# Optimization experiments

Measured on AMD Instinct MI355X. Metric: run time of the kernel, lower is better.

## Reference

```python
import jax, jax.numpy as jnp
import numpy as np

N = 100000
E = 1600000
IN_FEATS = 128
H_FEATS = 128
NUM_CLASSES = 64
BN_EPS = 1e-5


def setup_inputs() -> dict:
    key = jax.random.key(0)
    ks = jax.random.split(key, 16)
    inp = {
        "in_feat": jax.random.normal(ks[0], (N, IN_FEATS), dtype=jnp.float32),
        "src": jax.random.randint(ks[1], (E,), 0, N, dtype=jnp.int64),
        "dst": jax.random.randint(ks[2], (E,), 0, N, dtype=jnp.int64),
        # GraphConv weights (glorot-ish scale) and biases
        "W0": jax.random.normal(ks[3], (IN_FEATS, H_FEATS), dtype=jnp.float32) / np.sqrt(IN_FEATS),
        "b0": jnp.zeros((H_FEATS,), dtype=jnp.float32),
        "W1": jax.random.normal(ks[4], (H_FEATS, H_FEATS), dtype=jnp.float32) / np.sqrt(H_FEATS),
        "b1": jnp.zeros((H_FEATS,), dtype=jnp.float32),
        "W2": jax.random.normal(ks[5], (H_FEATS, NUM_CLASSES), dtype=jnp.float32) / np.sqrt(H_FEATS),
        "b2": jnp.zeros((NUM_CLASSES,), dtype=jnp.float32),
        # BatchNorm affine params
        "gamma0": jnp.ones((H_FEATS,), dtype=jnp.float32),
        "beta0": jnp.zeros((H_FEATS,), dtype=jnp.float32),
        "gamma1": jnp.ones((H_FEATS,), dtype=jnp.float32),
        "beta1": jnp.zeros((H_FEATS,), dtype=jnp.float32),
    }
    return inp


def _graph_conv(src, dst, h, W, b):
    # DGL GraphConv, norm='both': D_dst^{-1/2} A (D_src^{-1/2} h W) + b
    ones = jnp.ones((src.shape[0],), dtype=h.dtype)
    deg_out = jnp.clip(jax.ops.segment_sum(ones, src, num_segments=N), 1.0)
    deg_in = jnp.clip(jax.ops.segment_sum(ones, dst, num_segments=N), 1.0)
    h = h * jax.lax.rsqrt(deg_out)[:, None]
    h = h @ W  # mult weight before aggregation (same math either way)
    agg = jax.ops.segment_sum(h[src], dst, num_segments=N)  # SpMM
    return agg * jax.lax.rsqrt(deg_in)[:, None] + b


def _batch_norm(h, gamma, beta):
    # BatchNorm1d in training mode: biased batch stats over the node axis
    mean = jnp.mean(h, axis=0)
    var = jnp.mean(jnp.square(h - mean), axis=0)
    return (h - mean) * jax.lax.rsqrt(var + BN_EPS) * gamma + beta


def reference(in_feat, src, dst, W0, b0, W1, b1, W2, b2, gamma0, beta0, gamma1, beta1):
    h = _graph_conv(src, dst, in_feat, W0, b0)
    h = jax.nn.relu(_batch_norm(h, gamma0, beta0))  # dropout p=0 -> identity
    h = _graph_conv(src, dst, h, W1, b1)
    h = jax.nn.relu(_batch_norm(h, gamma1, beta1))
    return _graph_conv(src, dst, h, W2, b2)
```

## Files before the change

### kernel.cpp

```cpp
#include <hip/hip_runtime.h>

#define NFEAT 128
#define BT 2048
#define BSH 9
#define BSZ 512
#define NP 256

typedef __attribute__((ext_vector_type(8))) short short8v;
typedef __attribute__((ext_vector_type(4))) float float4v;

static inline size_t align_up(size_t x, size_t a) { return (x + a - 1) & ~(a - 1); }

__device__ inline unsigned short f2bf(float f) {
  unsigned u = __float_as_uint(f);
  u += 0x7FFF + ((u >> 16) & 1);
  return (unsigned short)(u >> 16);
}
__device__ inline unsigned pack2bf(float lo, float hi) {
  return ((unsigned)f2bf(lo)) | (((unsigned)f2bf(hi)) << 16);
}
__device__ inline float bflo(unsigned u) { return __uint_as_float(u << 16); }
__device__ inline float bfhi(unsigned u) { return __uint_as_float(u & 0xFFFF0000u); }
__device__ inline int goff(const int* __restrict__ off, const int* __restrict__ bscan, int i) {
  return off[i] + bscan[i >> 9];
}

__global__ __launch_bounds__(256) void k_bcount(const int* __restrict__ src,
                                                const int* __restrict__ dst,
                                                int* __restrict__ cnt, int E, int nb, int NBK) {
  __shared__ int hD[256], hS[256];
  const int t = threadIdx.x, b = blockIdx.x;
  hD[t] = 0; hS[t] = 0;
  __syncthreads();
  const int e0 = b * BT, e1 = min(E, e0 + BT);
  for (int e = e0 + t; e < e1; e += 256) {
    atomicAdd(&hD[dst[e] >> BSH], 1);
    atomicAdd(&hS[src[e] >> BSH], 1);
  }
  __syncthreads();
  if (t < NBK) {
    cnt[t * nb + b] = hD[t];
    cnt[(NBK + t) * nb + b] = hS[t];
  }
}

__global__ __launch_bounds__(512) void k_scanA(const int* __restrict__ in,
                                               int* __restrict__ out,
                                               int* __restrict__ bsum, int n) {
  __shared__ int tmp[512];
  const int t = threadIdx.x;
  const int i = blockIdx.x * 512 + t;
  int v = (i < n) ? in[i] : 0;
  tmp[t] = v;
  __syncthreads();
  for (int off = 1; off < 512; off <<= 1) {
    int y = (t >= off) ? tmp[t - off] : 0;
    __syncthreads();
    tmp[t] += y;
    __syncthreads();
  }
  int incl = tmp[t];
  if (i < n) out[i] = incl - v;
  if (t == 511) bsum[blockIdx.x] = incl;
}

__global__ __launch_bounds__(1024) void k_scanB(const int* __restrict__ bsum,
                                                int* __restrict__ bscan, int nb1) {
  __shared__ int tmp[1024];
  const int t = threadIdx.x;
  int v = (t < nb1) ? bsum[t] : 0;
  tmp[t] = v;
  __syncthreads();
  for (int off = 1; off < 1024; off <<= 1) {
    int y = (t >= off) ? tmp[t - off] : 0;
    __syncthreads();
    tmp[t] += y;
    __syncthreads();
  }
  bscan[t] = tmp[t] - v;
}

__global__ __launch_bounds__(256) void k_bplace(const int* __restrict__ src,
                                                const int* __restrict__ dst,
                                                const int* __restrict__ off,
                                                const int* __restrict__ bscan,
                                                int* __restrict__ buf, int E, int nb, int NBK) {
  __shared__ int cD[256], cS[256];
  const int t = threadIdx.x, b = blockIdx.x;
  if (t < NBK) {
    cD[t] = goff(off, bscan, t * nb + b);
    cS[t] = goff(off, bscan, (NBK + t) * nb + b);
  }
  __syncthreads();
  const int e0 = b * BT, e1 = min(E, e0 + BT);
  for (int e = e0 + t; e < e1; e += 256) {
    int s = src[e];
    int d = dst[e];
    int pD = atomicAdd(&cD[d >> BSH], 1);
    buf[pD] = ((d & (BSZ - 1)) << 17) | s;
    int pS = atomicAdd(&cS[s >> BSH], 1);
    buf[pS] = s;
  }
}

__global__ __launch_bounds__(256) void k_bcsr_deg(const int* __restrict__ buf,
                                                  const int* __restrict__ off,
                                                  const int* __restrict__ bscan,
                                                  int* __restrict__ row_ptr,
                                                  float* __restrict__ rsq_in,
                                                  float* __restrict__ rsq_out,
                                                  int* __restrict__ col,
                                                  int E, int nb, int NBK, int N) {
  const int k = blockIdx.x, t = threadIdx.x;
  __shared__ int cnt[BSZ];
  __shared__ int sc[BSZ];
  __shared__ int part[64];
  const int lo = goff(off, bscan, k * nb);
  const int hi = (k + 1 < NBK) ? goff(off, bscan, (k + 1) * nb) : E;
  cnt[t] = 0; cnt[t + 256] = 0;
  __syncthreads();
  for (int e = lo + t; e < hi; e += 256) atomicAdd(&cnt[((unsigned)buf[e]) >> 17], 1);
  __syncthreads();
  if (t < 64) {
    int r = 0;
#pragma unroll
    for (int j = 0; j < 8; ++j) r += cnt[t * 8 + j];
    part[t] = r;
  }
  __syncthreads();
  if (t == 0) {
    int run = 0;
    for (int i = 0; i < 64; ++i) { int v = part[i]; part[i] = run; run += v; }
  }
  __syncthreads();
  if (t < 64) {
    int run = part[t];
#pragma unroll
    for (int j = 0; j < 8; ++j) { int v = cnt[t * 8 + j]; sc[t * 8 + j] = run; run += v; }
  }
  __syncthreads();
  for (int idx = t; idx < BSZ; idx += 256) {
    int n = (k << BSH) + idx;
    if (n < N) {
      row_ptr[n] = lo + sc[idx];
      int c = cnt[idx]; if (c < 1) c = 1;
      rsq_in[n] = 1.0f / sqrtf((float)c);
    }
    cnt[idx] = sc[idx];
  }
  if (k == NBK - 1 && t == 0) row_ptr[N] = E;
  __syncthreads();
  for (int e = lo + t; e < hi; e += 256) {
    int w = buf[e];
    int p = atomicAdd(&cnt[((unsigned)w) >> 17], 1);
    col[lo + p] = w & 0x1FFFF;
  }
  __syncthreads();
  cnt[t] = 0; cnt[t + 256] = 0;
  __syncthreads();
  const int lo2 = goff(off, bscan, (NBK + k) * nb);
  const int hi2 = (k + 1 < NBK) ? goff(off, bscan, (NBK + k + 1) * nb) : 2 * E;
  for (int e = lo2 + t; e < hi2; e += 256) atomicAdd(&cnt[buf[e] & (BSZ - 1)], 1);
  __syncthreads();
  for (int idx = t; idx < BSZ; idx += 256) {
    int n = (k << BSH) + idx;
    if (n < N) {
      int c = cnt[idx]; if (c < 1) c = 1;
      rsq_out[n] = 1.0f / sqrtf((float)c);
    }
  }
}

__global__ __launch_bounds__(256) void k_wprep(const float* __restrict__ W0,
                                               const float* __restrict__ W1,
                                               const float* __restrict__ W2,
                                               unsigned short* __restrict__ Wt0,
                                               unsigned short* __restrict__ Wt1,
                                               unsigned short* __restrict__ Wt2) {
  int t = blockIdx.x * 256 + threadIdx.x;
  if (t < 16384) {
    int c = t >> 7, k = t & 127;
    Wt0[c * 128 + k] = f2bf(W0[k * 128 + c]);
  } else if (t < 32768) {
    int u = t - 16384;
    int c = u >> 7, k = u & 127;
    Wt1[c * 128 + k] = f2bf(W1[k * 128 + c]);
  } else if (t < 40960) {
    int u = t - 32768;
    int c = u >> 7, k = u & 127;
    Wt2[c * 128 + k] = f2bf(W2[k * 64 + c]);
  }
}

template <int CC>
__global__ __launch_bounds__(256) void k_gemm_mfma(
    const float* __restrict__ X32, const unsigned short* __restrict__ Xbf,
    const unsigned short* __restrict__ Wt,
    unsigned short* __restrict__ Ybf, const float* __restrict__ rsq_out,
    const float* __restrict__ bnscale, const float* __restrict__ bnshift,
    int Nrows, int mode) {
  constexpr int XBYTES = 64 * 256;
  constexpr int WBYTES = CC * 256;
  __shared__ __align__(16) char lds[XBYTES + WBYTES];
  const int tid = threadIdx.x;
  const int rowBase = blockIdx.x * 64;

  for (int u = tid; u < CC * 16; u += 256) {
    int c = u >> 4, kq = u & 15;
    uint4 v = *(const uint4*)(Wt + c * 128 + kq * 8);
    int byte = (c * 256 + kq * 16) ^ ((c & 7) << 4);
    *(uint4*)(&lds[XBYTES + byte]) = v;
  }
  if (mode == 0) {
#pragma unroll
    for (int i = 0; i < 8; ++i) {
      int u = tid + i * 256;
      int r = u >> 5, kq = u & 31;
      int gr = rowBase + r;
      float4 v = make_float4(0.f, 0.f, 0.f, 0.f);
      if (gr < Nrows) v = *(const float4*)(X32 + (size_t)gr * 128 + kq * 4);
      ushort4 o;
      o.x = f2bf(v.x); o.y = f2bf(v.y); o.z = f2bf(v.z); o.w = f2bf(v.w);
      int byte = (r * 256 + kq * 8) ^ ((r & 7) << 4);
      *(ushort4*)(&lds[byte]) = o;
    }
  } else {
#pragma unroll
    for (int i = 0; i < 4; ++i) {
      int u = tid + i * 256;
      int r = u >> 4, kq = u & 15;
      int gr = rowBase + r;
      uint4 v = make_uint4(0, 0, 0, 0);
      if (gr < Nrows) v = *(const uint4*)(Xbf + (size_t)gr * 128 + kq * 8);
      float f0 = bflo(v.x), f1 = bfhi(v.x), f2 = bflo(v.y), f3 = bfhi(v.y);
      float f4 = bflo(v.z), f5 = bfhi(v.z), f6 = bflo(v.w), f7 = bfhi(v.w);
      const float4 sA = *(const float4*)(bnscale + kq * 8);
      const float4 sB = *(const float4*)(bnscale + kq * 8 + 4);
      const float4 hA = *(const float4*)(bnshift + kq * 8);
      const float4 hB = *(const float4*)(bnshift + kq * 8 + 4);
      f0 = fmaxf(f0 * sA.x + hA.x, 0.f); f1 = fmaxf(f1 * sA.y + hA.y, 0.f);
      f2 = fmaxf(f2 * sA.z + hA.z, 0.f); f3 = fmaxf(f3 * sA.w + hA.w, 0.f);
      f4 = fmaxf(f4 * sB.x + hB.x, 0.f); f5 = fmaxf(f5 * sB.y + hB.y, 0.f);
      f6 = fmaxf(f6 * sB.z + hB.z, 0.f); f7 = fmaxf(f7 * sB.w + hB.w, 0.f);
      uint4 o;
      o.x = pack2bf(f0, f1); o.y = pack2bf(f2, f3);
      o.z = pack2bf(f4, f5); o.w = pack2bf(f6, f7);
      int byte = (r * 256 + kq * 16) ^ ((r & 7) << 4);
      *(uint4*)(&lds[byte]) = o;
    }
  }
  __syncthreads();

  const int wv = tid >> 6;
  const int l = tid & 63;
  const int l16 = l & 15, lk = l >> 4;

  short8v a[4];
  const int arow = wv * 16 + l16;
#pragma unroll
  for (int kk = 0; kk < 4; ++kk) {
    int byte = (arow * 256 + kk * 64 + lk * 16) ^ ((arow & 7) << 4);
    a[kk] = *(const short8v*)(&lds[byte]);
  }

  float4v acc[CC / 16];
#pragma unroll
  for (int ct = 0; ct < CC / 16; ++ct) acc[ct] = (float4v){0.f, 0.f, 0.f, 0.f};

#pragma unroll
  for (int ct = 0; ct < CC / 16; ++ct) {
    const int col = ct * 16 + l16;
#pragma unroll
    for (int kk = 0; kk < 4; ++kk) {
      int byte = XBYTES + ((col * 256 + kk * 64 + lk * 16) ^ ((col & 7) << 4));
      short8v b = *(const short8v*)(&lds[byte]);
      acc[ct] = __builtin_amdgcn_mfma_f32_16x16x32_bf16(a[kk], b, acc[ct], 0, 0, 0);
    }
  }

  const int row0 = rowBase + wv * 16 + lk * 4;
  float scr[4];
#pragma unroll
  for (int r = 0; r < 4; ++r) scr[r] = (row0 + r < Nrows) ? rsq_out[row0 + r] : 0.f;
#pragma unroll
  for (int ct = 0; ct < CC / 16; ++ct) {
#pragma unroll
    for (int r = 0; r < 4; ++r) {
      int row = row0 + r;
      if (row < Nrows)
        Ybf[(size_t)row * CC + ct * 16 + l16] = f2bf(acc[ct][r] * scr[r]);
    }
  }
}

template <int F, int OUT_BF>
__global__ __launch_bounds__(256) void k_spmm2(const int* __restrict__ row_ptr,
                                               const int* __restrict__ colidx,
                                               const unsigned short* __restrict__ xW,
                                               void* __restrict__ outv,
                                               const float* __restrict__ rsq_in,
                                               const float* __restrict__ bias, int Nrows) {
  constexpr int FL = F / 8;
  constexpr int G = 64 / FL;
  const int node = blockIdx.x * 4 + (threadIdx.x >> 6);
  if (node >= Nrows) return;
  const int l = threadIdx.x & 63;
  const int fl = l % FL, g = l / FL;
  const int e0 = row_ptr[node];
  const int e1 = row_ptr[node + 1];
  float acc[8] = {};
  int e = e0 + g;
  for (; e + 3 * G < e1; e += 4 * G) {
    int s0 = colidx[e];
    int s1 = colidx[e + G];
    int s2 = colidx[e + 2 * G];
    int s3 = colidx[e + 3 * G];
    uint4 v0 = *(const uint4*)&xW[(size_t)s0 * F + fl * 8];
    uint4 v1 = *(const uint4*)&xW[(size_t)s1 * F + fl * 8];
    uint4 v2 = *(const uint4*)&xW[(size_t)s2 * F + fl * 8];
    uint4 v3 = *(const uint4*)&xW[(size_t)s3 * F + fl * 8];
    acc[0] += bflo(v0.x); acc[1] += bfhi(v0.x); acc[2] += bflo(v0.y); acc[3] += bfhi(v0.y);
    acc[4] += bflo(v0.z); acc[5] += bfhi(v0.z); acc[6] += bflo(v0.w); acc[7] += bfhi(v0.w);
    acc[0] += bflo(v1.x); acc[1] += bfhi(v1.x); acc[2] += bflo(v1.y); acc[3] += bfhi(v1.y);
    acc[4] += bflo(v1.z); acc[5] += bfhi(v1.z); acc[6] += bflo(v1.w); acc[7] += bfhi(v1.w);
    acc[0] += bflo(v2.x); acc[1] += bfhi(v2.x); acc[2] += bflo(v2.y); acc[3] += bfhi(v2.y);
    acc[4] += bflo(v2.z); acc[5] += bfhi(v2.z); acc[6] += bflo(v2.w); acc[7] += bfhi(v2.w);
    acc[0] += bflo(v3.x); acc[1] += bfhi(v3.x); acc[2] += bflo(v3.y); acc[3] += bfhi(v3.y);
    acc[4] += bflo(v3.z); acc[5] += bfhi(v3.z); acc[6] += bflo(v3.w); acc[7] += bfhi(v3.w);
  }
  for (; e < e1; e += G) {
    int s0 = colidx[e];
    uint4 v0 = *(const uint4*)&xW[(size_t)s0 * F + fl * 8];
    acc[0] += bflo(v0.x); acc[1] += bfhi(v0.x); acc[2] += bflo(v0.y); acc[3] += bfhi(v0.y);
    acc[4] += bflo(v0.z); acc[5] += bfhi(v0.z); acc[6] += bflo(v0.w); acc[7] += bfhi(v0.w);
  }
#pragma unroll
  for (int m = FL; m < 64; m <<= 1) {
#pragma unroll
    for (int j = 0; j < 8; ++j) acc[j] += __shfl_xor(acc[j], m);
  }
  if (g != 0) return;
  const float sc = rsq_in[node];
  const float4 bA = *(const float4*)&bias[fl * 8];
  const float4 bB = *(const float4*)&bias[fl * 8 + 4];
  float o0 = acc[0] * sc + bA.x, o1 = acc[1] * sc + bA.y;
  float o2 = acc[2] * sc + bA.z, o3 = acc[3] * sc + bA.w;
  float o4 = acc[4] * sc + bB.x, o5 = acc[5] * sc + bB.y;
  float o6 = acc[6] * sc + bB.z, o7 = acc[7] * sc + bB.w;
  if (OUT_BF) {
    uint4 w;
    w.x = pack2bf(o0, o1); w.y = pack2bf(o2, o3);
    w.z = pack2bf(o4, o5); w.w = pack2bf(o6, o7);
    *(uint4*)&((unsigned short*)outv)[(size_t)node * F + fl * 8] = w;
  } else {
    float* out = (float*)outv;
    *(float4*)&out[(size_t)node * F + fl * 8] = make_float4(o0, o1, o2, o3);
    *(float4*)&out[(size_t)node * F + fl * 8 + 4] = make_float4(o4, o5, o6, o7);
  }
}

__global__ __launch_bounds__(256) void k_bn_stats_bf(const unsigned short* __restrict__ h,
                                                     float* __restrict__ psum,
                                                     float* __restrict__ pssq, int Nrows) {
  const int t = threadIdx.x;
  const int fs = t & 15;
  const int rg = t >> 4;
  float s[8] = {}, ss[8] = {};
  for (int r = blockIdx.x * 16 + rg; r < Nrows; r += gridDim.x * 16) {
    uint4 v = *(const uint4*)&h[(size_t)r * 128 + fs * 8];
    float f0 = bflo(v.x), f1 = bfhi(v.x), f2 = bflo(v.y), f3 = bfhi(v.y);
    float f4 = bflo(v.z), f5 = bfhi(v.z), f6 = bflo(v.w), f7 = bfhi(v.w);
    s[0] += f0; ss[0] += f0 * f0; s[1] += f1; ss[1] += f1 * f1;
    s[2] += f2; ss[2] += f2 * f2; s[3] += f3; ss[3] += f3 * f3;
    s[4] += f4; ss[4] += f4 * f4; s[5] += f5; ss[5] += f5 * f5;
    s[6] += f6; ss[6] += f6 * f6; s[7] += f7; ss[7] += f7 * f7;
  }
#pragma unroll
  for (int m = 16; m < 64; m <<= 1) {
#pragma unroll
    for (int j = 0; j < 8; ++j) { s[j] += __shfl_xor(s[j], m); ss[j] += __shfl_xor(ss[j], m); }
  }
  __shared__ float lsum[4][128], lssq[4][128];
  const int wv = t >> 6, wl = t & 63;
  if (wl < 16) {
#pragma unroll
    for (int j = 0; j < 8; ++j) { lsum[wv][wl * 8 + j] = s[j]; lssq[wv][wl * 8 + j] = ss[j]; }
  }
  __syncthreads();
  if (t < 128) {
    psum[(size_t)blockIdx.x * 128 + t] = lsum[0][t] + lsum[1][t] + lsum[2][t] + lsum[3][t];
    pssq[(size_t)blockIdx.x * 128 + t] = lssq[0][t] + lssq[1][t] + lssq[2][t] + lssq[3][t];
  }
}

__global__ __launch_bounds__(256) void k_bn_final(const float* __restrict__ psum,
                                                  const float* __restrict__ pssq,
                                                  const float* __restrict__ gamma,
                                                  const float* __restrict__ beta,
                                                  float* __restrict__ scale,
                                                  float* __restrict__ shift, int Nrows) {
  const int t = threadIdx.x;
  const int f = t & 127, half = t >> 7;
  float s = 0.f, ss = 0.f;
  for (int b = half * (NP / 2); b < (half + 1) * (NP / 2); ++b) {
    s += psum[(size_t)b * 128 + f];
    ss += pssq[(size_t)b * 128 + f];
  }
  __shared__ float ls[2][128], lss[2][128];
  ls[half][f] = s; lss[half][f] = ss;
  __syncthreads();
  if (t < 128) {
    float sum = ls[0][t] + ls[1][t];
    float sumsq = lss[0][t] + lss[1][t];
    float inv_n = 1.0f / (float)Nrows;
    float mean = sum * inv_n;
    float var = sumsq * inv_n - mean * mean;
    if (var < 0.f) var = 0.f;
    float sc = gamma[t] * (1.0f / sqrtf(var + 1e-5f));
    scale[t] = sc;
    shift[t] = beta[t] - mean * sc;
  }
}

extern "C" void kernel_launch(void* const* d_in, const int* in_sizes, int n_in,
                              void* d_out, int out_size, void* d_ws, size_t ws_size,
                              hipStream_t stream) {
  const float* in_feat = (const float*)d_in[0];
  const int* src = (const int*)d_in[1];
  const int* dst = (const int*)d_in[2];
  const float* W0 = (const float*)d_in[3];
  const float* b0 = (const float*)d_in[4];
  const float* W1 = (const float*)d_in[5];
  const float* b1 = (const float*)d_in[6];
  const float* W2 = (const float*)d_in[7];
  const float* b2 = (const float*)d_in[8];
  const float* gamma0 = (const float*)d_in[9];
  const float* beta0 = (const float*)d_in[10];
  const float* gamma1 = (const float*)d_in[11];
  const float* beta1 = (const float*)d_in[12];
  float* out = (float*)d_out;

  const int N = in_sizes[0] / NFEAT;
  const int E = in_sizes[1];

  const int nb = (E + BT - 1) / BT;
  const int NBK = (N + BSZ - 1) / BSZ;
  const int L = 2 * NBK * nb;
  const int nb1 = (L + 511) / 512;

  char* p = (char*)d_ws;
  auto carve = [&](size_t bytes) {
    char* q = p;
    p += align_up(bytes, 256);
    return q;
  };
  int* cnt = (int*)carve((size_t)L * 4);
  int* off = (int*)carve((size_t)L * 4);
  int* bsum = (int*)carve(1024 * 4);
  int* bscan = (int*)carve(1024 * 4);
  int* row_ptr = (int*)carve((size_t)(N + 1) * 4);
  int* col = (int*)carve((size_t)E * 4);
  float* rsq_out = (float*)carve((size_t)N * 4);
  float* rsq_in = (float*)carve((size_t)N * 4);
  float* psum0 = (float*)carve((size_t)NP * 128 * 4);
  float* pssq0 = (float*)carve((size_t)NP * 128 * 4);
  float* psum1 = (float*)carve((size_t)NP * 128 * 4);
  float* pssq1 = (float*)carve((size_t)NP * 128 * 4);
  float* bn_scale0 = (float*)carve(128 * 4);
  float* bn_shift0 = (float*)carve(128 * 4);
  float* bn_scale1 = (float*)carve(128 * 4);
  float* bn_shift1 = (float*)carve(128 * 4);
  unsigned short* Wt0 = (unsigned short*)carve(16384 * 2);
  unsigned short* Wt1 = (unsigned short*)carve(16384 * 2);
  unsigned short* Wt2 = (unsigned short*)carve(8192 * 2);
  unsigned short* xWbf = (unsigned short*)carve((size_t)N * NFEAT * 2);
  unsigned short* hbf = (unsigned short*)carve((size_t)N * NFEAT * 2);
  int* buf = (int*)carve((size_t)2 * E * 4);

  k_wprep<<<160, 256, 0, stream>>>(W0, W1, W2, Wt0, Wt1, Wt2);
  k_bcount<<<nb, 256, 0, stream>>>(src, dst, cnt, E, nb, NBK);
  k_scanA<<<nb1, 512, 0, stream>>>(cnt, off, bsum, L);
  k_scanB<<<1, 1024, 0, stream>>>(bsum, bscan, nb1);
  k_bplace<<<nb, 256, 0, stream>>>(src, dst, off, bscan, buf, E, nb, NBK);
  k_bcsr_deg<<<NBK, 256, 0, stream>>>(buf, off, bscan, row_ptr, rsq_in, rsq_out, col,
                                      E, nb, NBK, N);

  const int GR = (N + 63) / 64;
  const int GS = (N + 3) / 4;

  k_gemm_mfma<128><<<GR, 256, 0, stream>>>(in_feat, nullptr, Wt0, xWbf, rsq_out,
                                           nullptr, nullptr, N, 0);
  k_spmm2<128, 1><<<GS, 256, 0, stream>>>(row_ptr, col, xWbf, hbf, rsq_in, b0, N);
  k_bn_stats_bf<<<NP, 256, 0, stream>>>(hbf, psum0, pssq0, N);
  k_bn_final<<<1, 256, 0, stream>>>(psum0, pssq0, gamma0, beta0, bn_scale0, bn_shift0, N);

  k_gemm_mfma<128><<<GR, 256, 0, stream>>>(nullptr, hbf, Wt1, xWbf, rsq_out,
                                           bn_scale0, bn_shift0, N, 1);
  k_spmm2<128, 1><<<GS, 256, 0, stream>>>(row_ptr, col, xWbf, hbf, rsq_in, b1, N);
  k_bn_stats_bf<<<NP, 256, 0, stream>>>(hbf, psum1, pssq1, N);
  k_bn_final<<<1, 256, 0, stream>>>(psum1, pssq1, gamma1, beta1, bn_scale1, bn_shift1, N);

  k_gemm_mfma<64><<<GR, 256, 0, stream>>>(nullptr, hbf, Wt2, xWbf, rsq_out,
                                          bn_scale1, bn_shift1, N, 1);
  k_spmm2<64, 0><<<GS, 256, 0, stream>>>(row_ptr, col, xWbf, out, rsq_in, b2, N);
}
```

Baseline: 518.8 us.

## Cut launch count with global-atomic bucket bases and last-block BN finalize

Replaces the per-block count matrix and two-level scan with global atomic bucket totals, a single-block scan of bucket bases, and atomic cursor reservation in the placement kernel, which now recounts its own histogram. Weight prep is merged into the counting kernel, and the BN stats and finalize kernels become one kernel where the last block reduces the partials. Edge tile and BN partial counts are also changed. The aim is fewer kernel launches and less scan traffic, at the cost of nondeterministic bucket ordering, extra counting work in placement, and a memset.

```diff
diff --git a/kernel.cpp b/kernel.cpp
--- a/kernel.cpp
+++ b/kernel.cpp
@@ -1,10 +1,10 @@
 #include <hip/hip_runtime.h>
 
 #define NFEAT 128
-#define BT 2048
+#define BT 4096
 #define BSH 9
 #define BSZ 512
-#define NP 256
+#define NP 64
 
 typedef __attribute__((ext_vector_type(8))) short short8v;
 typedef __attribute__((ext_vector_type(4))) float float4v;
@@ -21,15 +21,36 @@
 }
 __device__ inline float bflo(unsigned u) { return __uint_as_float(u << 16); }
 __device__ inline float bfhi(unsigned u) { return __uint_as_float(u & 0xFFFF0000u); }
-__device__ inline int goff(const int* __restrict__ off, const int* __restrict__ bscan, int i) {
-  return off[i] + bscan[i >> 9];
-}
-
-__global__ __launch_bounds__(256) void k_bcount(const int* __restrict__ src,
-                                                const int* __restrict__ dst,
-                                                int* __restrict__ cnt, int E, int nb, int NBK) {
+
+__global__ __launch_bounds__(256) void k_prep(const float* __restrict__ W0,
+                                              const float* __restrict__ W1,
+                                              const float* __restrict__ W2,
+                                              unsigned short* __restrict__ Wt0,
+                                              unsigned short* __restrict__ Wt1,
+                                              unsigned short* __restrict__ Wt2,
+                                              const int* __restrict__ src,
+                                              const int* __restrict__ dst,
+                                              int* __restrict__ tot,
+                                              int E, int NBK) {
+  if (blockIdx.x < 160) {
+    int t = blockIdx.x * 256 + threadIdx.x;
+    if (t < 16384) {
+      int c = t >> 7, k = t & 127;
+      Wt0[c * 128 + k] = f2bf(W0[k * 128 + c]);
+    } else if (t < 32768) {
+      int u = t - 16384;
+      int c = u >> 7, k = u & 127;
+      Wt1[c * 128 + k] = f2bf(W1[k * 128 + c]);
+    } else if (t < 40960) {
+      int u = t - 32768;
+      int c = u >> 7, k = u & 127;
+      Wt2[c * 128 + k] = f2bf(W2[k * 64 + c]);
+    }
+    return;
+  }
+  const int b = blockIdx.x - 160;
   __shared__ int hD[256], hS[256];
-  const int t = threadIdx.x, b = blockIdx.x;
+  const int t = threadIdx.x;
   hD[t] = 0; hS[t] = 0;
   __syncthreads();
   const int e0 = b * BT, e1 = min(E, e0 + BT);
@@ -39,18 +60,19 @@
   }
   __syncthreads();
   if (t < NBK) {
-    cnt[t * nb + b] = hD[t];
-    cnt[(NBK + t) * nb + b] = hS[t];
-  }
-}
-
-__global__ __launch_bounds__(512) void k_scanA(const int* __restrict__ in,
-                                               int* __restrict__ out,
-                                               int* __restrict__ bsum, int n) {
+    if (hD[t]) atomicAdd(&tot[t], hD[t]);
+    if (hS[t]) atomicAdd(&tot[NBK + t], hS[t]);
+  }
+}
+
+__global__ __launch_bounds__(512) void k_bases(const int* __restrict__ tot,
+                                               int* __restrict__ base,
+                                               int* __restrict__ cursor,
+                                               int E, int NBK) {
   __shared__ int tmp[512];
   const int t = threadIdx.x;
-  const int i = blockIdx.x * 512 + t;
-  int v = (i < n) ? in[i] : 0;
+  const int n = 2 * NBK;
+  int v = (t < n) ? tot[t] : 0;
   tmp[t] = v;
   __syncthreads();
   for (int off = 1; off < 512; off <<= 1) {
@@ -59,64 +81,58 @@
     tmp[t] += y;
     __syncthreads();
   }
-  int incl = tmp[t];
-  if (i < n) out[i] = incl - v;
-  if (t == 511) bsum[blockIdx.x] = incl;
-}
-
-__global__ __launch_bounds__(1024) void k_scanB(const int* __restrict__ bsum,
-                                                int* __restrict__ bscan, int nb1) {
-  __shared__ int tmp[1024];
-  const int t = threadIdx.x;
-  int v = (t < nb1) ? bsum[t] : 0;
-  tmp[t] = v;
-  __syncthreads();
-  for (int off = 1; off < 1024; off <<= 1) {
-    int y = (t >= off) ? tmp[t - off] : 0;
-    __syncthreads();
-    tmp[t] += y;
-    __syncthreads();
-  }
-  bscan[t] = tmp[t] - v;
+  if (t < n) {
+    int b = tmp[t] - v;
+    base[t] = b;
+    cursor[t] = b;
+  }
+  if (t == 0) base[n] = 2 * E;
 }
 
 __global__ __launch_bounds__(256) void k_bplace(const int* __restrict__ src,
                                                 const int* __restrict__ dst,
-                                                const int* __restrict__ off,
-                                                const int* __restrict__ bscan,
-                                                int* __restrict__ buf, int E, int nb, int NBK) {
-  __shared__ int cD[256], cS[256];
+                                                int* __restrict__ cursor,
+                                                int* __restrict__ buf, int E, int NBK) {
+  __shared__ int hD[256], hS[256];
   const int t = threadIdx.x, b = blockIdx.x;
+  hD[t] = 0; hS[t] = 0;
+  __syncthreads();
+  const int e0 = b * BT, e1 = min(E, e0 + BT);
+  for (int e = e0 + t; e < e1; e += 256) {
+    atomicAdd(&hD[dst[e] >> BSH], 1);
+    atomicAdd(&hS[src[e] >> BSH], 1);
+  }
+  __syncthreads();
   if (t < NBK) {
-    cD[t] = goff(off, bscan, t * nb + b);
-    cS[t] = goff(off, bscan, (NBK + t) * nb + b);
-  }
-  __syncthreads();
-  const int e0 = b * BT, e1 = min(E, e0 + BT);
+    int c = hD[t];
+    hD[t] = c ? atomicAdd(&cursor[t], c) : 0;
+    c = hS[t];
+    hS[t] = c ? atomicAdd(&cursor[NBK + t], c) : 0;
+  }
+  __syncthreads();
   for (int e = e0 + t; e < e1; e += 256) {
     int s = src[e];
     int d = dst[e];
-    int pD = atomicAdd(&cD[d >> BSH], 1);
+    int pD = atomicAdd(&hD[d >> BSH], 1);
     buf[pD] = ((d & (BSZ - 1)) << 17) | s;
-    int pS = atomicAdd(&cS[s >> BSH], 1);
+    int pS = atomicAdd(&hS[s >> BSH], 1);
     buf[pS] = s;
   }
 }
 
 __global__ __launch_bounds__(256) void k_bcsr_deg(const int* __restrict__ buf,
-                                                  const int* __restrict__ off,
-                                                  const int* __restrict__ bscan,
+                                                  const int* __restrict__ base,
                                                   int* __restrict__ row_ptr,
                                                   float* __restrict__ rsq_in,
                                                   float* __restrict__ rsq_out,
                                                   int* __restrict__ col,
-                                                  int E, int nb, int NBK, int N) {
+                                                  int E, int NBK, int N) {
   const int k = blockIdx.x, t = threadIdx.x;
   __shared__ int cnt[BSZ];
   __shared__ int sc[BSZ];
   __shared__ int part[64];
-  const int lo = goff(off, bscan, k * nb);
-  const int hi = (k + 1 < NBK) ? goff(off, bscan, (k + 1) * nb) : E;
+  const int lo = base[k];
+  const int hi = base[k + 1];
   cnt[t] = 0; cnt[t + 256] = 0;
   __syncthreads();
   for (int e = lo + t; e < hi; e += 256) atomicAdd(&cnt[((unsigned)buf[e]) >> 17], 1);
@@ -158,8 +174,8 @@
   __syncthreads();
   cnt[t] = 0; cnt[t + 256] = 0;
   __syncthreads();
-  const int lo2 = goff(off, bscan, (NBK + k) * nb);
-  const int hi2 = (k + 1 < NBK) ? goff(off, bscan, (NBK + k + 1) * nb) : 2 * E;
+  const int lo2 = base[NBK + k];
+  const int hi2 = base[NBK + k + 1];
   for (int e = lo2 + t; e < hi2; e += 256) atomicAdd(&cnt[buf[e] & (BSZ - 1)], 1);
   __syncthreads();
   for (int idx = t; idx < BSZ; idx += 256) {
@@ -168,27 +184,6 @@
       int c = cnt[idx]; if (c < 1) c = 1;
       rsq_out[n] = 1.0f / sqrtf((float)c);
     }
-  }
-}
-
-__global__ __launch_bounds__(256) void k_wprep(const float* __restrict__ W0,
-                                               const float* __restrict__ W1,
-                                               const float* __restrict__ W2,
-                                               unsigned short* __restrict__ Wt0,
-                                               unsigned short* __restrict__ Wt1,
-                                               unsigned short* __restrict__ Wt2) {
-  int t = blockIdx.x * 256 + threadIdx.x;
-  if (t < 16384) {
-    int c = t >> 7, k = t & 127;
-    Wt0[c * 128 + k] = f2bf(W0[k * 128 + c]);
-  } else if (t < 32768) {
-    int u = t - 16384;
-    int c = u >> 7, k = u & 127;
-    Wt1[c * 128 + k] = f2bf(W1[k * 128 + c]);
-  } else if (t < 40960) {
-    int u = t - 32768;
-    int c = u >> 7, k = u & 127;
-    Wt2[c * 128 + k] = f2bf(W2[k * 64 + c]);
   }
 }
 
@@ -359,9 +354,14 @@
   }
 }
 
-__global__ __launch_bounds__(256) void k_bn_stats_bf(const unsigned short* __restrict__ h,
-                                                     float* __restrict__ psum,
-                                                     float* __restrict__ pssq, int Nrows) {
+__global__ __launch_bounds__(256) void k_bn_fused(const unsigned short* __restrict__ h,
+                                                  float* __restrict__ psum,
+                                                  float* __restrict__ pssq,
+                                                  int* __restrict__ done,
+                                                  const float* __restrict__ gamma,
+                                                  const float* __restrict__ beta,
+                                                  float* __restrict__ scale,
+                                                  float* __restrict__ shift, int Nrows) {
   const int t = threadIdx.x;
   const int fs = t & 15;
   const int rg = t >> 4;
@@ -391,27 +391,18 @@
     psum[(size_t)blockIdx.x * 128 + t] = lsum[0][t] + lsum[1][t] + lsum[2][t] + lsum[3][t];
     pssq[(size_t)blockIdx.x * 128 + t] = lssq[0][t] + lssq[1][t] + lssq[2][t] + lssq[3][t];
   }
-}
-
-__global__ __launch_bounds__(256) void k_bn_final(const float* __restrict__ psum,
-                                                  const float* __restrict__ pssq,
-                                                  const float* __restrict__ gamma,
-                                                  const float* __restrict__ beta,
-                                                  float* __restrict__ scale,
-                                                  float* __restrict__ shift, int Nrows) {
-  const int t = threadIdx.x;
-  const int f = t & 127, half = t >> 7;
-  float s = 0.f, ss = 0.f;
-  for (int b = half * (NP / 2); b < (half + 1) * (NP / 2); ++b) {
-    s += psum[(size_t)b * 128 + f];
-    ss += pssq[(size_t)b * 128 + f];
-  }
-  __shared__ float ls[2][128], lss[2][128];
-  ls[half][f] = s; lss[half][f] = ss;
-  __syncthreads();
+  __shared__ int amLast;
+  __threadfence();
+  __syncthreads();
+  if (t == 0) amLast = (atomicAdd(done, 1) == (int)gridDim.x - 1);
+  __syncthreads();
+  if (!amLast) return;
   if (t < 128) {
-    float sum = ls[0][t] + ls[1][t];
-    float sumsq = lss[0][t] + lss[1][t];
+    float sum = 0.f, sumsq = 0.f;
+    for (int b = 0; b < NP; ++b) {
+      sum += psum[(size_t)b * 128 + t];
+      sumsq += pssq[(size_t)b * 128 + t];
+    }
     float inv_n = 1.0f / (float)Nrows;
     float mean = sum * inv_n;
     float var = sumsq * inv_n - mean * mean;
@@ -445,8 +436,6 @@
 
   const int nb = (E + BT - 1) / BT;
   const int NBK = (N + BSZ - 1) / BSZ;
-  const int L = 2 * NBK * nb;
-  const int nb1 = (L + 511) / 512;
 
   char* p = (char*)d_ws;
   auto carve = [&](size_t bytes) {
@@ -454,10 +443,11 @@
     p += align_up(bytes, 256);
     return q;
   };
-  int* cnt = (int*)carve((size_t)L * 4);
-  int* off = (int*)carve((size_t)L * 4);
-  int* bsum = (int*)carve(1024 * 4);
-  int* bscan = (int*)carve(1024 * 4);
+  int* tot = (int*)carve((512 + 2) * 4);
+  int* done0 = tot + 512;
+  int* done1 = tot + 513;
+  int* base = (int*)carve(520 * 4);
+  int* cursor = (int*)carve(520 * 4);
   int* row_ptr = (int*)carve((size_t)(N + 1) * 4);
   int* col = (int*)carve((size_t)E * 4);
   float* rsq_out = (float*)carve((size_t)N * 4);
@@ -477,13 +467,12 @@
   unsigned short* hbf = (unsigned short*)carve((size_t)N * NFEAT * 2);
   int* buf = (int*)carve((size_t)2 * E * 4);
 
-  k_wprep<<<160, 256, 0, stream>>>(W0, W1, W2, Wt0, Wt1, Wt2);
-  k_bcount<<<nb, 256, 0, stream>>>(src, dst, cnt, E, nb, NBK);
-  k_scanA<<<nb1, 512, 0, stream>>>(cnt, off, bsum, L);
-  k_scanB<<<1, 1024, 0, stream>>>(bsum, bscan, nb1);
-  k_bplace<<<nb, 256, 0, stream>>>(src, dst, off, bscan, buf, E, nb, NBK);
-  k_bcsr_deg<<<NBK, 256, 0, stream>>>(buf, off, bscan, row_ptr, rsq_in, rsq_out, col,
-                                      E, nb, NBK, N);
+  hipMemsetAsync(tot, 0, (512 + 2) * 4, stream);
+
+  k_prep<<<160 + nb, 256, 0, stream>>>(W0, W1, W2, Wt0, Wt1, Wt2, src, dst, tot, E, NBK);
+  k_bases<<<1, 512, 0, stream>>>(tot, base, cursor, E, NBK);
+  k_bplace<<<nb, 256, 0, stream>>>(src, dst, cursor, buf, E, NBK);
+  k_bcsr_deg<<<NBK, 256, 0, stream>>>(buf, base, row_ptr, rsq_in, rsq_out, col, E, NBK, N);
 
   const int GR = (N + 63) / 64;
   const int GS = (N + 3) / 4;
@@ -491,14 +480,14 @@
   k_gemm_mfma<128><<<GR, 256, 0, stream>>>(in_feat, nullptr, Wt0, xWbf, rsq_out,
                                            nullptr, nullptr, N, 0);
   k_spmm2<128, 1><<<GS, 256, 0, stream>>>(row_ptr, col, xWbf, hbf, rsq_in, b0, N);
-  k_bn_stats_bf<<<NP, 256, 0, stream>>>(hbf, psum0, pssq0, N);
-  k_bn_final<<<1, 256, 0, stream>>>(psum0, pssq0, gamma0, beta0, bn_scale0, bn_shift0, N);
+  k_bn_fused<<<NP, 256, 0, stream>>>(hbf, psum0, pssq0, done0, gamma0, beta0,
+                                     bn_scale0, bn_shift0, N);
 
   k_gemm_mfma<128><<<GR, 256, 0, stream>>>(nullptr, hbf, Wt1, xWbf, rsq_out,
                                            bn_scale0, bn_shift0, N, 1);
   k_spmm2<128, 1><<<GS, 256, 0, stream>>>(row_ptr, col, xWbf, hbf, rsq_in, b1, N);
-  k_bn_stats_bf<<<NP, 256, 0, stream>>>(hbf, psum1, pssq1, N);
-  k_bn_final<<<1, 256, 0, stream>>>(psum1, pssq1, gamma1, beta1, bn_scale1, bn_shift1, N);
+  k_bn_fused<<<NP, 256, 0, stream>>>(hbf, psum1, pssq1, done1, gamma1, beta1,
+                                     bn_scale1, bn_shift1, N);
 
   k_gemm_mfma<64><<<GR, 256, 0, stream>>>(nullptr, hbf, Wt2, xWbf, rsq_out,
                                           bn_scale1, bn_shift1, N, 1);
```

Result: no change. 519.1 us (+0.1%).
